# Performance work log

Hardware: AMD Instinct MI355X
Metric: run time of the kernel (lower is better)

## Reference

```python
import jax, jax.numpy as jnp
import numpy as np
import math

WS = 12          # window side
N = WS * WS      # tokens per window = 144
C = 384          # channels
H = 12           # heads
NW = 4           # num windows per image (mask dim)
BW = 512         # total windows (num_windows * B)


def _rel_tables():
    # log-spaced continuous relative coords table, shape ((2*WS-1)^2, 2)
    r = np.arange(-(WS - 1), WS, dtype=np.float32)
    rc = np.stack(np.meshgrid(r, r, indexing='ij'), axis=-1)  # (2W-1, 2W-1, 2)
    rc = rc / (WS - 1) * WS
    table = np.sign(rc) * np.log2(np.abs(rc) + 1.0) / np.log2(8.0)
    # pairwise relative position index, shape (N, N)
    c = np.stack(np.meshgrid(np.arange(WS), np.arange(WS), indexing='ij')).reshape(2, -1)
    rel = (c[:, :, None] - c[:, None, :]).transpose(1, 2, 0)  # (N, N, 2)
    rel[..., 0] += WS - 1
    rel[..., 1] += WS - 1
    rel[..., 0] *= 2 * WS - 1
    idx = rel.sum(-1)
    return jnp.asarray(table.reshape(-1, 2)), jnp.asarray(idx)


def setup_inputs() -> dict:
    key = jax.random.key(0)
    ks = jax.random.split(key, 8)
    return {
        'x': jax.random.normal(ks[0], (BW, N, C), jnp.float32),
        'mask': jax.random.normal(ks[1], (NW, N, N), jnp.float32),
        'qkv_w': jax.random.normal(ks[2], (3 * C, C), jnp.float32) * 0.02,
        'qkv_b': jnp.zeros((3 * C,), jnp.float32),
        'logit_scale': jnp.log(10.0) * jnp.ones((H, 1, 1), jnp.float32),
        'cpb_w1': jax.random.normal(ks[3], (512, 2), jnp.float32) * 0.02,
        'cpb_b1': jnp.zeros((512,), jnp.float32),
        'cpb_w2': jax.random.normal(ks[4], (H, 512), jnp.float32) * 0.02,
        'proj_w': jax.random.normal(ks[5], (C, C), jnp.float32) * 0.02,
        'proj_b': jnp.zeros((C,), jnp.float32),
    }


def _l2norm(t):
    # F.normalize(dim=-1): divide by L2 norm clamped at 1e-12
    n = jnp.sqrt(jnp.sum(t * t, axis=-1, keepdims=True))
    return t / jnp.maximum(n, 1e-12)


def reference(x, mask, qkv_w, qkv_b, logit_scale, cpb_w1, cpb_b1, cpb_w2, proj_w, proj_b):
    table, idx = _rel_tables()
    B_, Nn, Cc = x.shape
    hd = Cc // H
    qkv = (x @ qkv_w.T + qkv_b).reshape(B_, Nn, 3, H, hd).transpose(2, 0, 3, 1, 4)
    q, k, v = qkv[0], qkv[1], qkv[2]  # each (B_, H, N, hd)

    # cosine attention with learned, clamped logit scale
    attn = jnp.einsum('bhnd,bhmd->bhnm', _l2norm(q), _l2norm(k))
    scale = jnp.exp(jnp.minimum(logit_scale, math.log(1.0 / 0.01)))  # (H,1,1)
    attn = attn * scale[None]

    # CPB-MLP relative position bias
    bias_tab = jax.nn.relu(table @ cpb_w1.T + cpb_b1) @ cpb_w2.T  # (529, H)
    bias = bias_tab[idx.reshape(-1)].reshape(Nn, Nn, H).transpose(2, 0, 1)
    attn = attn + 16.0 * jax.nn.sigmoid(bias)[None]

    # shifted-window mask add, then softmax
    num_win = mask.shape[0]
    attn = attn.reshape(B_ // num_win, num_win, H, Nn, Nn) + mask[None, :, None]
    attn = jax.nn.softmax(attn.reshape(B_, H, Nn, Nn), axis=-1)

    out = jnp.einsum('bhnm,bhmd->bnhd', attn, v).reshape(B_, Nn, Cc)
    return out @ proj_w.T + proj_b
```

## Files before the change

### kernel.cpp

```cpp
#include <hip/hip_runtime.h>
#include <hip/hip_fp16.h>


typedef _Float16 half8 __attribute__((ext_vector_type(8)));
typedef _Float16 half4v __attribute__((ext_vector_type(4)));
typedef float floatx4 __attribute__((ext_vector_type(4)));

#define BW 512
#define NTOK 144
#define CDIM 384
#define NH 12
#define HD 32
#define MROWS (BW * NTOK)
#define QKVN (3 * CDIM)
#define NCASTB (MROWS * CDIM / 8 / 256)
#define NWB 288

__device__ inline void llds16(const void* g, void* l) {
    __builtin_amdgcn_global_load_lds((const __attribute__((address_space(1))) void*)g,
                                     (__attribute__((address_space(3))) void*)l, 16, 0, 0);
}

__device__ inline void cstore(_Float16* p, float v) { *p = (_Float16)v; }
__device__ inline void cstore(float* p, float v) { __builtin_nontemporal_store(v, p); }

__global__ __launch_bounds__(256) void prep(const float* __restrict__ x,
                                            _Float16* __restrict__ xh,
                                            const float* __restrict__ w_qkv,
                                            _Float16* __restrict__ qh,
                                            const float* __restrict__ w_proj,
                                            _Float16* __restrict__ ph,
                                            const float* __restrict__ w1,
                                            const float* __restrict__ b1,
                                            const float* __restrict__ w2,
                                            float* __restrict__ tab) {
    __shared__ float red[4][12];
    const int b = blockIdx.x;
    const int j = threadIdx.x;

    if (b < NCASTB) {
        int i = b * 256 + j;
        const float4* s4 = (const float4*)x;
        float4 a = s4[2 * i], c = s4[2 * i + 1];
        half8 h;
        h[0] = (_Float16)a.x; h[1] = (_Float16)a.y; h[2] = (_Float16)a.z; h[3] = (_Float16)a.w;
        h[4] = (_Float16)c.x; h[5] = (_Float16)c.y; h[6] = (_Float16)c.z; h[7] = (_Float16)c.w;
        ((half8*)xh)[i] = h;
        return;
    }
    if (b < NCASTB + NWB) {
        const int nq = QKVN * CDIM / 8;
        int i = (b - NCASTB) * 256 + j;
        const float4* s4; half8* d8; int k;
        if (i < nq) { s4 = (const float4*)w_qkv; d8 = (half8*)qh; k = i; }
        else        { s4 = (const float4*)w_proj; d8 = (half8*)ph; k = i - nq; }
        float4 a = s4[2 * k], c = s4[2 * k + 1];
        half8 h;
        h[0] = (_Float16)a.x; h[1] = (_Float16)a.y; h[2] = (_Float16)a.z; h[3] = (_Float16)a.w;
        h[4] = (_Float16)c.x; h[5] = (_Float16)c.y; h[6] = (_Float16)c.z; h[7] = (_Float16)c.w;
        d8[k] = h;
        return;
    }
    const int t = b - (NCASTB + NWB);
    float u0 = (float)((t / 23) - 11) * (12.0f / 11.0f);
    float u1 = (float)((t % 23) - 11) * (12.0f / 11.0f);
    float x0 = copysignf(log2f(fabsf(u0) + 1.0f) * (1.0f / 3.0f), u0);
    float x1 = copysignf(log2f(fabsf(u1) + 1.0f) * (1.0f / 3.0f), u1);

    float acc[12] = {};
#pragma unroll
    for (int half = 0; half < 2; half++) {
        const int jj = j + half * 256;
        float hj = fmaf(x0, w1[2 * jj], fmaf(x1, w1[2 * jj + 1], b1[jj]));
        hj = fmaxf(hj, 0.0f);
#pragma unroll
        for (int q = 0; q < 12; q++) acc[q] += hj * w2[q * 512 + jj];
    }
#pragma unroll
    for (int q = 0; q < 12; q++) {
        acc[q] += __shfl_xor(acc[q], 1);  acc[q] += __shfl_xor(acc[q], 2);
        acc[q] += __shfl_xor(acc[q], 4);  acc[q] += __shfl_xor(acc[q], 8);
        acc[q] += __shfl_xor(acc[q], 16); acc[q] += __shfl_xor(acc[q], 32);
    }
    const int wv = j >> 6, l = j & 63;
    if (l == 0) {
#pragma unroll
        for (int q = 0; q < 12; q++) red[wv][q] = acc[q];
    }
    __syncthreads();
    if (j < 12) tab[t * 12 + j] = red[0][j] + red[1][j] + red[2][j] + red[3][j];
}

__global__ __launch_bounds__(256) void build_cm(const float* __restrict__ mask,
                                                const float* __restrict__ tab,
                                                float* __restrict__ CM) {
    int e = blockIdx.x * 256 + threadIdx.x;
    if (e >= 4 * NH * NTOK * NTOK) return;
    int j = e % NTOK; int r1 = e / NTOK;
    int i = r1 % NTOK; int r2 = r1 / NTOK;
    int h = r2 % NH;   int m = r2 / NH;
    int rt = ((i / 12) - (j / 12) + 11) * 23 + ((i % 12) - (j % 12) + 11);
    float bv = tab[rt * 12 + h];
    CM[e] = mask[m * (NTOK * NTOK) + i * NTOK + j] + 16.0f / (1.0f + __expf(-bv));
}

template <typename OutT>
__global__ __launch_bounds__(512) void gemm_bt(const _Float16* __restrict__ A,
                                               const _Float16* __restrict__ B,
                                               const float* __restrict__ bias,
                                               OutT* __restrict__ C, int M, int N, int K) {
    __shared__ __align__(16) _Float16 As[3][256 * 32];
    __shared__ __align__(16) _Float16 Bs[3][128 * 32];
    const int t = threadIdx.x;
    const int wv = t >> 6, l = t & 63;
    const int wm = wv >> 1, wn = wv & 1;
    const int lr = l & 15, lk = l >> 4;

    const int ntn = N >> 7;
    const int t8 = gridDim.x >> 3;
    const int tile = (blockIdx.x & 7) * t8 + (blockIdx.x >> 3);
    const long m0 = (long)(tile / ntn) * 256, n0 = (long)(tile % ntn) * 128;

    const int srow = t >> 2;
    const int scol = ((t & 3) ^ ((srow >> 1) & 3)) * 8;
    const _Float16* ag = A + (m0 + srow) * (long)K + scol;
    const _Float16* bg = B + (n0 + srow) * (long)K + scol;

    floatx4 acc[4][4] = {};
    const int nk = K >> 5;
    const int aoff = wm * 64 + lr, boff = wn * 64 + lr;
    const int lka = (lk ^ ((lr >> 1) & 3)) * 8;

    llds16(ag,                  &As[0][t * 8]);
    llds16(ag + 128 * (long)K,  &As[0][t * 8 + 4096]);
    llds16(bg,                  &Bs[0][t * 8]);
    ag += 32; bg += 32;
    llds16(ag,                  &As[1][t * 8]);
    llds16(ag + 128 * (long)K,  &As[1][t * 8 + 4096]);
    llds16(bg,                  &Bs[1][t * 8]);
    ag += 32; bg += 32;

    int cur = 0, nx2 = 2;
    for (int it = 0; it < nk - 1; ++it) {
        asm volatile("s_waitcnt vmcnt(3)" ::: "memory");
        __builtin_amdgcn_s_barrier();
        __builtin_amdgcn_sched_barrier(0);

        if (it + 2 < nk) {
            llds16(ag,                 &As[nx2][t * 8]);
            llds16(ag + 128 * (long)K, &As[nx2][t * 8 + 4096]);
            llds16(bg,                 &Bs[nx2][t * 8]);
            ag += 32; bg += 32;
        }

        half8 af[4], bf[4];
#pragma unroll
        for (int fi = 0; fi < 4; fi++)
            af[fi] = *(const half8*)&As[cur][(aoff + fi * 16) * 32 + lka];
#pragma unroll
        for (int fj = 0; fj < 4; fj++)
            bf[fj] = *(const half8*)&Bs[cur][(boff + fj * 16) * 32 + lka];
#pragma unroll
        for (int fi = 0; fi < 4; fi++)
#pragma unroll
            for (int fj = 0; fj < 4; fj++)
                acc[fi][fj] = __builtin_amdgcn_mfma_f32_16x16x32_f16(af[fi], bf[fj], acc[fi][fj], 0, 0, 0);

        cur = (cur == 2) ? 0 : cur + 1;
        nx2 = (nx2 == 2) ? 0 : nx2 + 1;
    }

    {
        asm volatile("s_waitcnt vmcnt(0)" ::: "memory");
        __builtin_amdgcn_s_barrier();
        __builtin_amdgcn_sched_barrier(0);
        half8 af[4], bf[4];
#pragma unroll
        for (int fi = 0; fi < 4; fi++)
            af[fi] = *(const half8*)&As[cur][(aoff + fi * 16) * 32 + lka];
#pragma unroll
        for (int fj = 0; fj < 4; fj++)
            bf[fj] = *(const half8*)&Bs[cur][(boff + fj * 16) * 32 + lka];
#pragma unroll
        for (int fi = 0; fi < 4; fi++)
#pragma unroll
            for (int fj = 0; fj < 4; fj++)
                acc[fi][fj] = __builtin_amdgcn_mfma_f32_16x16x32_f16(af[fi], bf[fj], acc[fi][fj], 0, 0, 0);
    }

#pragma unroll
    for (int fi = 0; fi < 4; fi++) {
        const long row = m0 + wm * 64 + fi * 16 + lk * 4;
#pragma unroll
        for (int fj = 0; fj < 4; fj++) {
            const long col = n0 + wn * 64 + fj * 16 + lr;
            const float bv = bias[col];
#pragma unroll
            for (int r = 0; r < 4; r++) {
                float v = acc[fi][fj][r] + bv;
                cstore(&C[(row + r) * (long)N + col], v);
            }
        }
    }
}

__global__ __launch_bounds__(576) void attn_win(const _Float16* __restrict__ qkv,
                                                const float* __restrict__ CM,
                                                const float* __restrict__ lscale,
                                                _Float16* __restrict__ O) {
    __shared__ __align__(16) _Float16 Kn[NTOK * HD];
    __shared__ __align__(16) _Float16 Vt[HD * NTOK];

    const int per = gridDim.x >> 3;
    const int bid = (blockIdx.x & 7) * per + (blockIdx.x >> 3);
    const int w = bid / NH, h = bid % NH;
    const int t = threadIdx.x;
    const int wv = t >> 6, l = t & 63;
    const int lr = l & 15, lk = l >> 4;

    const float sc = expf(fminf(lscale[h], 4.6051701859880914f));

    {
        const int row = t >> 2, part = t & 3;
        const size_t base = (size_t)(w * NTOK + row) * QKVN + h * HD + part * 8;
        half8 kv = *(const half8*)(qkv + base + CDIM);
        float ss = 0.f;
#pragma unroll
        for (int j = 0; j < 8; j++) { float f = (float)kv[j]; ss += f * f; }
        ss += __shfl_xor(ss, 1); ss += __shfl_xor(ss, 2);
        float inv = 1.0f / fmaxf(sqrtf(ss), 1e-12f);
        half8 kn;
#pragma unroll
        for (int j = 0; j < 8; j++) kn[j] = (_Float16)((float)kv[j] * inv);
        *(half8*)&Kn[row * HD + part * 8] = kn;

        half8 vv = *(const half8*)(qkv + base + 2 * CDIM);
#pragma unroll
        for (int j = 0; j < 8; j++) Vt[(part * 8 + j) * NTOK + row] = vv[j];
    }

    half8 aq;
    {
        const size_t qb = (size_t)(w * NTOK + wv * 16 + lr) * QKVN + h * HD + lk * 8;
        half8 q = *(const half8*)(qkv + qb);
        float ss = 0.f;
#pragma unroll
        for (int j = 0; j < 8; j++) { float f = (float)q[j]; ss += f * f; }
        ss += __shfl_xor(ss, 16); ss += __shfl_xor(ss, 32);
        float inv = sc / fmaxf(sqrtf(ss), 1e-12f);
#pragma unroll
        for (int j = 0; j < 8; j++) aq[j] = (_Float16)((float)q[j] * inv);
    }
    __syncthreads();

    floatx4 s[9];
#pragma unroll
    for (int cj = 0; cj < 9; cj++) {
        half8 bk = *(const half8*)&Kn[(cj * 16 + lr) * HD + lk * 8];
        floatx4 z = {};
        s[cj] = __builtin_amdgcn_mfma_f32_16x16x32_f16(bk, aq, z, 0, 0, 0);
    }
    const float* cmb = CM + (size_t)((w & 3) * NH + h) * (NTOK * NTOK)
                     + (size_t)(wv * 16 + lr) * NTOK + lk * 4;
#pragma unroll
    for (int cj = 0; cj < 9; cj++) {
        float4 c4 = *(const float4*)(cmb + cj * 16);
        s[cj][0] += c4.x; s[cj][1] += c4.y; s[cj][2] += c4.z; s[cj][3] += c4.w;
    }

    float m = s[0][0];
#pragma unroll
    for (int cj = 0; cj < 9; cj++)
#pragma unroll
        for (int r = 0; r < 4; r++) m = fmaxf(m, s[cj][r]);
    m = fmaxf(m, __shfl_xor(m, 16)); m = fmaxf(m, __shfl_xor(m, 32));
    float sum = 0.f;
#pragma unroll
    for (int cj = 0; cj < 9; cj++)
#pragma unroll
        for (int r = 0; r < 4; r++) { s[cj][r] = __expf(s[cj][r] - m); sum += s[cj][r]; }
    sum += __shfl_xor(sum, 16); sum += __shfl_xor(sum, 32);
    const float inv = 1.0f / sum;

    half4v pa[9];
#pragma unroll
    for (int cj = 0; cj < 9; cj++) {
        pa[cj][0] = (_Float16)s[cj][0]; pa[cj][1] = (_Float16)s[cj][1];
        pa[cj][2] = (_Float16)s[cj][2]; pa[cj][3] = (_Float16)s[cj][3];
    }

    floatx4 o0 = {}, o1 = {};
#pragma unroll
    for (int cj = 0; cj < 9; cj++) {
        half4v v0 = *(const half4v*)&Vt[lr * NTOK + cj * 16 + lk * 4];
        half4v v1 = *(const half4v*)&Vt[(16 + lr) * NTOK + cj * 16 + lk * 4];
        o0 = __builtin_amdgcn_mfma_f32_16x16x16f16(v0, pa[cj], o0, 0, 0, 0);
        o1 = __builtin_amdgcn_mfma_f32_16x16x16f16(v1, pa[cj], o1, 0, 0, 0);
    }

    const size_t ob = (size_t)(w * NTOK + wv * 16 + lr) * CDIM + h * HD + lk * 4;
    half4v r0, r1;
#pragma unroll
    for (int r = 0; r < 4; r++) {
        r0[r] = (_Float16)(o0[r] * inv);
        r1[r] = (_Float16)(o1[r] * inv);
    }
    *(half4v*)&O[ob] = r0;
    *(half4v*)&O[ob + 16] = r1;
}

extern "C" void kernel_launch(void* const* d_in, const int* in_sizes, int n_in,
                              void* d_out, int out_size, void* d_ws, size_t ws_size,
                              hipStream_t stream) {
    const float* x     = (const float*)d_in[0];
    const float* mask  = (const float*)d_in[1];
    const float* qkv_w = (const float*)d_in[2];
    const float* qkv_b = (const float*)d_in[3];
    const float* lsc   = (const float*)d_in[4];
    const float* cw1   = (const float*)d_in[5];
    const float* cb1   = (const float*)d_in[6];
    const float* cw2   = (const float*)d_in[7];
    const float* pw    = (const float*)d_in[8];
    const float* pb    = (const float*)d_in[9];
    (void)in_sizes; (void)n_in; (void)out_size; (void)ws_size;

    char* ws = (char*)d_ws;
    float*    tab  = (float*)(ws);
    float*    CM   = (float*)(ws + 25600);
    _Float16* qw_h = (_Float16*)(ws + 4006912);
    _Float16* pw_h = (_Float16*)(ws + 4891648);
    _Float16* x_h  = (_Float16*)(ws + 5186560);
    _Float16* qkvh = (_Float16*)(ws + 61809664);
    _Float16* o_h  = x_h;

    prep<<<NCASTB + NWB + 529, 256, 0, stream>>>(
        x, x_h, qkv_w, qw_h, pw, pw_h, cw1, cb1, cw2, tab);
    build_cm<<<(4 * NH * NTOK * NTOK + 255) / 256, 256, 0, stream>>>(mask, tab, CM);

    gemm_bt<_Float16><<<(QKVN / 128) * (MROWS / 256), 512, 0, stream>>>(
        x_h, qw_h, qkv_b, qkvh, MROWS, QKVN, CDIM);

    attn_win<<<BW * NH, 576, 0, stream>>>(qkvh, CM, lsc, o_h);

    gemm_bt<float><<<(CDIM / 128) * (MROWS / 256), 512, 0, stream>>>(
        o_h, pw_h, pb, (float*)d_out, MROWS, CDIM, CDIM);
}
```

Measured before the change: 432.6 us.

## Fuse QKV projection GEMM into per-window attention kernel

Removes the separate QKV GEMM and its fp16 qkv intermediate. A new kernel runs one block per window and loops over all 12 heads. For each head it computes that head's Q/K/V slice with MFMA from x and weight tiles, staged into LDS through a triple-buffered global_load_lds pipeline with XOR-swizzled layouts, then runs the same cosine attention. This avoids writing and re-reading the large qkv buffer, but the grid shrinks to only 512 blocks, which may underfill the GPU and serialize the heads within each block.

```diff
diff --git a/kernel.cpp b/kernel.cpp
--- a/kernel.cpp
+++ b/kernel.cpp
@@ -204,109 +204,164 @@
     }
 }
 
-__global__ __launch_bounds__(576) void attn_win(const _Float16* __restrict__ qkv,
+__global__ __launch_bounds__(576) void qkv_attn(const _Float16* __restrict__ xh,
+                                                const _Float16* __restrict__ qw,
+                                                const float* __restrict__ qb,
                                                 const float* __restrict__ CM,
                                                 const float* __restrict__ lscale,
                                                 _Float16* __restrict__ O) {
-    __shared__ __align__(16) _Float16 Kn[NTOK * HD];
-    __shared__ __align__(16) _Float16 Vt[HD * NTOK];
+    __shared__ __align__(16) _Float16 XT[3][NTOK * 32];
+    __shared__ __align__(16) _Float16 WSL[3][96 * 32];
+    __shared__ __align__(16) _Float16 QS[NTOK * 32];
+    __shared__ __align__(16) _Float16 KN[NTOK * 32];
+    __shared__ __align__(16) _Float16 VT[HD * NTOK];
 
     const int per = gridDim.x >> 3;
-    const int bid = (blockIdx.x & 7) * per + (blockIdx.x >> 3);
-    const int w = bid / NH, h = bid % NH;
+    const int w = (blockIdx.x & 7) * per + (blockIdx.x >> 3);
     const int t = threadIdx.x;
     const int wv = t >> 6, l = t & 63;
     const int lr = l & 15, lk = l >> 4;
-
-    const float sc = expf(fminf(lscale[h], 4.6051701859880914f));
-
-    {
-        const int row = t >> 2, part = t & 3;
-        const size_t base = (size_t)(w * NTOK + row) * QKVN + h * HD + part * 8;
-        half8 kv = *(const half8*)(qkv + base + CDIM);
-        float ss = 0.f;
-#pragma unroll
-        for (int j = 0; j < 8; j++) { float f = (float)kv[j]; ss += f * f; }
-        ss += __shfl_xor(ss, 1); ss += __shfl_xor(ss, 2);
-        float inv = 1.0f / fmaxf(sqrtf(ss), 1e-12f);
-        half8 kn;
-#pragma unroll
-        for (int j = 0; j < 8; j++) kn[j] = (_Float16)((float)kv[j] * inv);
-        *(half8*)&Kn[row * HD + part * 8] = kn;
-
-        half8 vv = *(const half8*)(qkv + base + 2 * CDIM);
-#pragma unroll
-        for (int j = 0; j < 8; j++) Vt[(part * 8 + j) * NTOK + row] = vv[j];
-    }
-
-    half8 aq;
-    {
-        const size_t qb = (size_t)(w * NTOK + wv * 16 + lr) * QKVN + h * HD + lk * 8;
-        half8 q = *(const half8*)(qkv + qb);
-        float ss = 0.f;
-#pragma unroll
-        for (int j = 0; j < 8; j++) { float f = (float)q[j]; ss += f * f; }
-        ss += __shfl_xor(ss, 16); ss += __shfl_xor(ss, 32);
-        float inv = sc / fmaxf(sqrtf(ss), 1e-12f);
-#pragma unroll
-        for (int j = 0; j < 8; j++) aq[j] = (_Float16)((float)q[j] * inv);
-    }
-    __syncthreads();
-
-    floatx4 s[9];
-#pragma unroll
-    for (int cj = 0; cj < 9; cj++) {
-        half8 bk = *(const half8*)&Kn[(cj * 16 + lr) * HD + lk * 8];
-        floatx4 z = {};
-        s[cj] = __builtin_amdgcn_mfma_f32_16x16x32_f16(bk, aq, z, 0, 0, 0);
-    }
-    const float* cmb = CM + (size_t)((w & 3) * NH + h) * (NTOK * NTOK)
-                     + (size_t)(wv * 16 + lr) * NTOK + lk * 4;
-#pragma unroll
-    for (int cj = 0; cj < 9; cj++) {
-        float4 c4 = *(const float4*)(cmb + cj * 16);
-        s[cj][0] += c4.x; s[cj][1] += c4.y; s[cj][2] += c4.z; s[cj][3] += c4.w;
-    }
-
-    float m = s[0][0];
-#pragma unroll
-    for (int cj = 0; cj < 9; cj++)
-#pragma unroll
-        for (int r = 0; r < 4; r++) m = fmaxf(m, s[cj][r]);
-    m = fmaxf(m, __shfl_xor(m, 16)); m = fmaxf(m, __shfl_xor(m, 32));
-    float sum = 0.f;
-#pragma unroll
-    for (int cj = 0; cj < 9; cj++)
-#pragma unroll
-        for (int r = 0; r < 4; r++) { s[cj][r] = __expf(s[cj][r] - m); sum += s[cj][r]; }
-    sum += __shfl_xor(sum, 16); sum += __shfl_xor(sum, 32);
-    const float inv = 1.0f / sum;
-
-    half4v pa[9];
-#pragma unroll
-    for (int cj = 0; cj < 9; cj++) {
-        pa[cj][0] = (_Float16)s[cj][0]; pa[cj][1] = (_Float16)s[cj][1];
-        pa[cj][2] = (_Float16)s[cj][2]; pa[cj][3] = (_Float16)s[cj][3];
-    }
-
-    floatx4 o0 = {}, o1 = {};
-#pragma unroll
-    for (int cj = 0; cj < 9; cj++) {
-        half4v v0 = *(const half4v*)&Vt[lr * NTOK + cj * 16 + lk * 4];
-        half4v v1 = *(const half4v*)&Vt[(16 + lr) * NTOK + cj * 16 + lk * 4];
-        o0 = __builtin_amdgcn_mfma_f32_16x16x16f16(v0, pa[cj], o0, 0, 0, 0);
-        o1 = __builtin_amdgcn_mfma_f32_16x16x16f16(v1, pa[cj], o1, 0, 0, 0);
-    }
-
-    const size_t ob = (size_t)(w * NTOK + wv * 16 + lr) * CDIM + h * HD + lk * 4;
-    half4v r0, r1;
-#pragma unroll
-    for (int r = 0; r < 4; r++) {
-        r0[r] = (_Float16)(o0[r] * inv);
-        r1[r] = (_Float16)(o1[r] * inv);
-    }
-    *(half4v*)&O[ob] = r0;
-    *(half4v*)&O[ob + 16] = r1;
+    const int lka = (lk ^ ((lr >> 1) & 3)) * 8;
+
+    const int srow = t >> 2, sx = ((t & 3) ^ ((srow >> 1) & 3)) * 8;
+    const _Float16* xsrc = xh + ((size_t)w * NTOK + srow) * CDIM + sx;
+    const _Float16* wsrc = qw + ((size_t)(srow >> 5) * CDIM + (srow & 31)) * CDIM + sx;
+
+    auto STAGE = [&](int gg) {
+        const int hh = gg / 12, kk = gg - hh * 12, sl = gg % 3;
+        llds16(xsrc + kk * 32, &XT[sl][t * 8]);
+        if (t < 384) llds16(wsrc + hh * (32 * CDIM) + kk * 32, &WSL[sl][t * 8]);
+    };
+
+    const int xoff = (wv * 16 + lr) * 32 + lka;
+    const int woffb = lr * 32 + lka;
+
+    STAGE(0); STAGE(1);
+
+    for (int h = 0; h < NH; ++h) {
+        const float sc = expf(fminf(lscale[h], 4.6051701859880914f));
+        floatx4 acc[6] = {};
+
+        for (int kc = 0; kc < 12; ++kc) {
+            const int g = h * 12 + kc;
+            __syncthreads();
+            if (g + 2 < 144) STAGE(g + 2);
+
+            const _Float16* xs = XT[g % 3];
+            const _Float16* wl = WSL[g % 3];
+            half8 af = *(const half8*)&xs[xoff];
+#pragma unroll
+            for (int dt = 0; dt < 6; ++dt) {
+                half8 bf = *(const half8*)&wl[woffb + dt * 512];
+                acc[dt] = __builtin_amdgcn_mfma_f32_16x16x32_f16(af, bf, acc[dt], 0, 0, 0);
+            }
+        }
+
+        const int tokb = wv * 16 + lk * 4;
+#pragma unroll
+        for (int dt = 0; dt < 6; ++dt) {
+            const float bv = qb[(dt >> 1) * CDIM + h * HD + (dt & 1) * 16 + lr];
+#pragma unroll
+            for (int r = 0; r < 4; ++r) {
+                const float v = acc[dt][r] + bv;
+                const int tok = tokb + r;
+                const int fs = (tok >> 1) & 3;
+                if (dt < 2) {
+                    const int dim = dt * 16 + lr;
+                    QS[tok * 32 + (((dim >> 3) ^ fs) << 3) + (dim & 7)] = (_Float16)v;
+                } else if (dt < 4) {
+                    const int dim = (dt - 2) * 16 + lr;
+                    KN[tok * 32 + (((dim >> 3) ^ fs) << 3) + (dim & 7)] = (_Float16)v;
+                } else {
+                    VT[((dt - 4) * 16 + lr) * NTOK + tok] = (_Float16)v;
+                }
+            }
+        }
+        __syncthreads();
+
+        {
+            const int row = t >> 2, part = t & 3;
+            _Float16* kp = &KN[row * 32 + ((part ^ ((row >> 1) & 3)) << 3)];
+            half8 kv = *(const half8*)kp;
+            float ss = 0.f;
+#pragma unroll
+            for (int j = 0; j < 8; j++) { float f = (float)kv[j]; ss += f * f; }
+            ss += __shfl_xor(ss, 1); ss += __shfl_xor(ss, 2);
+            const float inv = 1.0f / fmaxf(sqrtf(ss), 1e-12f);
+            half8 kn;
+#pragma unroll
+            for (int j = 0; j < 8; j++) kn[j] = (_Float16)((float)kv[j] * inv);
+            *(half8*)kp = kn;
+        }
+        __syncthreads();
+
+        half8 aq;
+        {
+            half8 q = *(const half8*)&QS[xoff];
+            float ss = 0.f;
+#pragma unroll
+            for (int j = 0; j < 8; j++) { float f = (float)q[j]; ss += f * f; }
+            ss += __shfl_xor(ss, 16); ss += __shfl_xor(ss, 32);
+            const float inv = sc / fmaxf(sqrtf(ss), 1e-12f);
+#pragma unroll
+            for (int j = 0; j < 8; j++) aq[j] = (_Float16)((float)q[j] * inv);
+        }
+
+        floatx4 s[9];
+#pragma unroll
+        for (int cj = 0; cj < 9; cj++) {
+            half8 bk = *(const half8*)&KN[cj * 512 + woffb];
+            floatx4 z = {};
+            s[cj] = __builtin_amdgcn_mfma_f32_16x16x32_f16(bk, aq, z, 0, 0, 0);
+        }
+        const float* cmb = CM + (size_t)((w & 3) * NH + h) * (NTOK * NTOK)
+                         + (size_t)(wv * 16 + lr) * NTOK + lk * 4;
+#pragma unroll
+        for (int cj = 0; cj < 9; cj++) {
+            float4 c4 = *(const float4*)(cmb + cj * 16);
+            s[cj][0] += c4.x; s[cj][1] += c4.y; s[cj][2] += c4.z; s[cj][3] += c4.w;
+        }
+
+        float m = s[0][0];
+#pragma unroll
+        for (int cj = 0; cj < 9; cj++)
+#pragma unroll
+            for (int r = 0; r < 4; r++) m = fmaxf(m, s[cj][r]);
+        m = fmaxf(m, __shfl_xor(m, 16)); m = fmaxf(m, __shfl_xor(m, 32));
+        float sum = 0.f;
+#pragma unroll
+        for (int cj = 0; cj < 9; cj++)
+#pragma unroll
+            for (int r = 0; r < 4; r++) { s[cj][r] = __expf(s[cj][r] - m); sum += s[cj][r]; }
+        sum += __shfl_xor(sum, 16); sum += __shfl_xor(sum, 32);
+        const float inv = 1.0f / sum;
+
+        half4v pa[9];
+#pragma unroll
+        for (int cj = 0; cj < 9; cj++) {
+            pa[cj][0] = (_Float16)s[cj][0]; pa[cj][1] = (_Float16)s[cj][1];
+            pa[cj][2] = (_Float16)s[cj][2]; pa[cj][3] = (_Float16)s[cj][3];
+        }
+
+        floatx4 o0 = {}, o1 = {};
+#pragma unroll
+        for (int cj = 0; cj < 9; cj++) {
+            half4v v0 = *(const half4v*)&VT[lr * NTOK + cj * 16 + lk * 4];
+            half4v v1 = *(const half4v*)&VT[(16 + lr) * NTOK + cj * 16 + lk * 4];
+            o0 = __builtin_amdgcn_mfma_f32_16x16x16f16(v0, pa[cj], o0, 0, 0, 0);
+            o1 = __builtin_amdgcn_mfma_f32_16x16x16f16(v1, pa[cj], o1, 0, 0, 0);
+        }
+
+        const size_t ob = ((size_t)w * NTOK + wv * 16 + lr) * CDIM + h * HD + lk * 4;
+        half4v r0, r1;
+#pragma unroll
+        for (int r = 0; r < 4; r++) {
+            r0[r] = (_Float16)(o0[r] * inv);
+            r1[r] = (_Float16)(o1[r] * inv);
+        }
+        *(half4v*)&O[ob] = r0;
+        *(half4v*)&O[ob + 16] = r1;
+    }
 }
 
 extern "C" void kernel_launch(void* const* d_in, const int* in_sizes, int n_in,
@@ -330,17 +385,13 @@
     _Float16* qw_h = (_Float16*)(ws + 4006912);
     _Float16* pw_h = (_Float16*)(ws + 4891648);
     _Float16* x_h  = (_Float16*)(ws + 5186560);
-    _Float16* qkvh = (_Float16*)(ws + 61809664);
-    _Float16* o_h  = x_h;
+    _Float16* o_h  = (_Float16*)(ws + 61809664);
 
     prep<<<NCASTB + NWB + 529, 256, 0, stream>>>(
         x, x_h, qkv_w, qw_h, pw, pw_h, cw1, cb1, cw2, tab);
     build_cm<<<(4 * NH * NTOK * NTOK + 255) / 256, 256, 0, stream>>>(mask, tab, CM);
 
-    gemm_bt<_Float16><<<(QKVN / 128) * (MROWS / 256), 512, 0, stream>>>(
-        x_h, qw_h, qkv_b, qkvh, MROWS, QKVN, CDIM);
-
-    attn_win<<<BW * NH, 576, 0, stream>>>(qkvh, CM, lsc, o_h);
+    qkv_attn<<<BW, 576, 0, stream>>>(x_h, qw_h, qkv_b, CM, lsc, o_h);
 
     gemm_bt<float><<<(CDIM / 128) * (MROWS / 256), 512, 0, stream>>>(
         o_h, pw_h, pb, (float*)d_out, MROWS, CDIM, CDIM);
```

After: 539.4 us. +24.7%, slower.
